# Performance work log

Measured on AMD Instinct MI355X. Metric: run time of the kernel, lower is better.

Reference implementation:

```python
import jax, jax.numpy as jnp
import numpy as np

THRESH = 0.5
DECAY = 0.25


def setup_inputs() -> dict:
    key = jax.random.key(0)
    x = jax.random.normal(key, (8, 32, 128, 32, 32), dtype=jnp.float32)
    return {"x": x}


def reference(x) -> jnp.ndarray:
    # LIF membrane recurrence over leading time axis.
    # mem[0] = x[0]; mem[i] = decay * mem[i-1] * (1 - spike[i-1]) + x[i]
    # spike[i] = (mem[i] > thresh)
    def step(carry, x_t):
        mem_old, spike_prev = carry
        mem = mem_old * DECAY * (1.0 - spike_prev) + x_t
        spike = (mem > THRESH).astype(x_t.dtype)
        return (mem, spike), spike

    zeros = jnp.zeros_like(x[0])
    _, spikes = jax.lax.scan(step, (zeros, zeros), x)
    return spikes
```

## Files before the change

kernel.cpp:

```cpp
#include <hip/hip_runtime.h>


#define LIF_T 8
#define LIF_N (32 * 128 * 32 * 32)
#define LIF_N4 (LIF_N / 4)

typedef float f32x4 __attribute__((ext_vector_type(4)));

__global__ __launch_bounds__(256) void lif_kernel(
    const f32x4* __restrict__ x4, f32x4* __restrict__ o4) {
    const int i = blockIdx.x * 256 + threadIdx.x;

    f32x4 xs[LIF_T];
#pragma unroll
    for (int t = 0; t < LIF_T; ++t) {
        xs[t] = x4[(size_t)t * LIF_N4 + i];
    }
    __builtin_amdgcn_sched_barrier(0);

    float mx = 0.f, my = 0.f, mz = 0.f, mw = 0.f;
    float sx = 0.f, sy = 0.f, sz = 0.f, sw = 0.f;

#pragma unroll
    for (int t = 0; t < LIF_T; ++t) {
        const float dx = (sx != 0.f) ? 0.f : 0.25f;
        const float dy = (sy != 0.f) ? 0.f : 0.25f;
        const float dz = (sz != 0.f) ? 0.f : 0.25f;
        const float dw = (sw != 0.f) ? 0.f : 0.25f;
        mx = mx * dx + xs[t].x;
        my = my * dy + xs[t].y;
        mz = mz * dz + xs[t].z;
        mw = mw * dw + xs[t].w;
        sx = (mx > 0.5f) ? 1.f : 0.f;
        sy = (my > 0.5f) ? 1.f : 0.f;
        sz = (mz > 0.5f) ? 1.f : 0.f;
        sw = (mw > 0.5f) ? 1.f : 0.f;
        f32x4 s;
        s.x = sx; s.y = sy; s.z = sz; s.w = sw;
        __builtin_nontemporal_store(s, &o4[(size_t)t * LIF_N4 + i]);
    }
}

extern "C" void kernel_launch(void* const* d_in, const int* in_sizes, int n_in,
                              void* d_out, int out_size, void* d_ws, size_t ws_size,
                              hipStream_t stream) {
    const f32x4* x4 = (const f32x4*)d_in[0];
    f32x4* o4 = (f32x4*)d_out;
    const int blocks = LIF_N4 / 256;
    lif_kernel<<<blocks, 256, 0, stream>>>(x4, o4);
}
```

Before: 241.7 us.

## Process four vec4 columns per thread with double-buffered time-step loads

The launch shrinks to 1024 blocks, and each thread now handles four strided float4 columns, covering all elements (LIF_N4 = 4*NTHREADS). Loads for the next time step are issued in a ping-pong register buffer while the current step is computed and stored, so fewer registers are held than when all eight steps were loaded up front. Stores are now plain stores instead of nontemporal ones, which may change cache behaviour. The intent is to cut per-block overhead and keep memory requests in flight with a steady load/compute/store pipeline.

```diff
diff --git a/kernel.cpp b/kernel.cpp
--- a/kernel.cpp
+++ b/kernel.cpp
@@ -4,41 +4,64 @@
 #define LIF_T 8
 #define LIF_N (32 * 128 * 32 * 32)
 #define LIF_N4 (LIF_N / 4)
+#define NTHREADS (1024 * 256)
+#define SSTRIDE NTHREADS
 
 typedef float f32x4 __attribute__((ext_vector_type(4)));
+
+__device__ __forceinline__ f32x4 lif_step(f32x4& m, f32x4& s, const f32x4 v) {
+    m.x = m.x * ((s.x != 0.f) ? 0.f : 0.25f) + v.x;
+    m.y = m.y * ((s.y != 0.f) ? 0.f : 0.25f) + v.y;
+    m.z = m.z * ((s.z != 0.f) ? 0.f : 0.25f) + v.z;
+    m.w = m.w * ((s.w != 0.f) ? 0.f : 0.25f) + v.w;
+    s.x = (m.x > 0.5f) ? 1.f : 0.f;
+    s.y = (m.y > 0.5f) ? 1.f : 0.f;
+    s.z = (m.z > 0.5f) ? 1.f : 0.f;
+    s.w = (m.w > 0.5f) ? 1.f : 0.f;
+    return s;
+}
 
 __global__ __launch_bounds__(256) void lif_kernel(
     const f32x4* __restrict__ x4, f32x4* __restrict__ o4) {
     const int i = blockIdx.x * 256 + threadIdx.x;
+    const f32x4* __restrict__ xp = x4 + i;
+    f32x4* __restrict__ op = o4 + i;
 
-    f32x4 xs[LIF_T];
-#pragma unroll
-    for (int t = 0; t < LIF_T; ++t) {
-        xs[t] = x4[(size_t)t * LIF_N4 + i];
-    }
-    __builtin_amdgcn_sched_barrier(0);
+    f32x4 a0, a1, a2, a3, b0, b1, b2, b3;
+    f32x4 m0 = {0,0,0,0}, m1 = {0,0,0,0}, m2 = {0,0,0,0}, m3 = {0,0,0,0};
+    f32x4 s0 = {0,0,0,0}, s1 = {0,0,0,0}, s2 = {0,0,0,0}, s3 = {0,0,0,0};
 
-    float mx = 0.f, my = 0.f, mz = 0.f, mw = 0.f;
-    float sx = 0.f, sy = 0.f, sz = 0.f, sw = 0.f;
+#define LOAD4(B, t)                                                        \
+    B##0 = xp[(size_t)(t) * LIF_N4 + 0 * SSTRIDE];                         \
+    B##1 = xp[(size_t)(t) * LIF_N4 + 1 * SSTRIDE];                         \
+    B##2 = xp[(size_t)(t) * LIF_N4 + 2 * SSTRIDE];                         \
+    B##3 = xp[(size_t)(t) * LIF_N4 + 3 * SSTRIDE];                         \
+    asm volatile("" : "+v"(B##0), "+v"(B##1), "+v"(B##2), "+v"(B##3));
 
-#pragma unroll
-    for (int t = 0; t < LIF_T; ++t) {
-        const float dx = (sx != 0.f) ? 0.f : 0.25f;
-        const float dy = (sy != 0.f) ? 0.f : 0.25f;
-        const float dz = (sz != 0.f) ? 0.f : 0.25f;
-        const float dw = (sw != 0.f) ? 0.f : 0.25f;
-        mx = mx * dx + xs[t].x;
-        my = my * dy + xs[t].y;
-        mz = mz * dz + xs[t].z;
-        mw = mw * dw + xs[t].w;
-        sx = (mx > 0.5f) ? 1.f : 0.f;
-        sy = (my > 0.5f) ? 1.f : 0.f;
-        sz = (mz > 0.5f) ? 1.f : 0.f;
-        sw = (mw > 0.5f) ? 1.f : 0.f;
-        f32x4 s;
-        s.x = sx; s.y = sy; s.z = sz; s.w = sw;
-        __builtin_nontemporal_store(s, &o4[(size_t)t * LIF_N4 + i]);
-    }
+#define STEP4(B, t)                                                        \
+    op[(size_t)(t) * LIF_N4 + 0 * SSTRIDE] = lif_step(m0, s0, B##0);       \
+    op[(size_t)(t) * LIF_N4 + 1 * SSTRIDE] = lif_step(m1, s1, B##1);       \
+    op[(size_t)(t) * LIF_N4 + 2 * SSTRIDE] = lif_step(m2, s2, B##2);       \
+    op[(size_t)(t) * LIF_N4 + 3 * SSTRIDE] = lif_step(m3, s3, B##3);
+
+    LOAD4(a, 0)
+    LOAD4(b, 1)
+    STEP4(a, 0)
+    LOAD4(a, 2)
+    STEP4(b, 1)
+    LOAD4(b, 3)
+    STEP4(a, 2)
+    LOAD4(a, 4)
+    STEP4(b, 3)
+    LOAD4(b, 5)
+    STEP4(a, 4)
+    LOAD4(a, 6)
+    STEP4(b, 5)
+    LOAD4(b, 7)
+    STEP4(a, 6)
+    STEP4(b, 7)
+#undef LOAD4
+#undef STEP4
 }
 
 extern "C" void kernel_launch(void* const* d_in, const int* in_sizes, int n_in,
@@ -46,6 +69,5 @@
                               hipStream_t stream) {
     const f32x4* x4 = (const f32x4*)d_in[0];
     f32x4* o4 = (f32x4*)d_out;
-    const int blocks = LIF_N4 / 256;
-    lif_kernel<<<blocks, 256, 0, stream>>>(x4, o4);
+    lif_kernel<<<1024, 256, 0, stream>>>(x4, o4);
 }
```

Result: faster. 234.6 us (-2.9%).
